# Kernel optimization log

Measured on AMD Instinct MI355X. Metric: run time of the kernel, lower is better.

Reference implementation:

```python
import jax, jax.numpy as jnp
import numpy as np

# irreps_in = irreps_out = "32x0e + 16x1o"; irreps_edge = "1x0e + 1x1o"
N_SCAL, N_VEC = 32, 16
RADIAL_EMBED, HIDDEN = 64, 64
# FullyConnectedTensorProduct instructions (uvw), v == 1 since edge mults are 1:
#  P1: 0e x 0e -> 0e (32*32)   P2: 1o x 1o -> 0e (16*32)
#  P3: 0e x 1o -> 1o (32*16)   P4: 1o x 0e -> 1o (16*16)   P5: 1o x 1o -> 1o (16*16)
SPLITS = np.cumsum([0, 32 * 32, 16 * 32, 32 * 16, 16 * 16, 16 * 16])
W_NUMEL = int(SPLITS[-1])  # 2560
SILU_NORM = 1.6790425  # e3nn normalize2mom constant for silu
# path weights: alpha = ir_out.dim / sum(num_elements over paths into same output)
PW0 = (1.0 / (32.0 + 16.0)) ** 0.5          # scalar output paths
PW1 = (3.0 / (32.0 + 16.0 + 16.0)) ** 0.5   # vector output paths
INV_SQRT3 = 3.0 ** -0.5  # wigner_3j(0,1,1)/(1,0,1)/(1,1,0) magnitude
INV_SQRT6 = 6.0 ** -0.5  # wigner_3j(1,1,1) = eps_ijk / sqrt(6)
N_NODES, N_EDGES = 8192, 65536


def radial_net(e, W0, W1, W2):
    # e3nn FullyConnectedNet: x @ (W / sqrt(fan_in)), normalized silu between layers
    h = e
    for W in (W0, W1):
        h = jax.nn.silu(h @ (W / jnp.sqrt(jnp.float32(W.shape[0])))) * SILU_NORM
    return h @ (W2 / jnp.sqrt(jnp.float32(W2.shape[0])))


def setup_inputs() -> dict:
    key = jax.random.key(0)
    ks = jax.random.split(key, 9)
    edge_index = jax.random.randint(ks[0], (2, N_EDGES), 0, N_NODES)
    node_feat = jax.random.normal(ks[1], (N_NODES, N_SCAL + 3 * N_VEC), jnp.float32)
    edge_feat = jax.random.normal(ks[2], (N_EDGES, 4), jnp.float32)
    edge_embed = jax.random.normal(ks[3], (N_EDGES, RADIAL_EMBED), jnp.float32)
    W_fc0 = jax.random.normal(ks[4], (RADIAL_EMBED, HIDDEN), jnp.float32)
    W_fc1 = jax.random.normal(ks[5], (HIDDEN, HIDDEN), jnp.float32)
    W_fc2 = jax.random.normal(ks[6], (HIDDEN, W_NUMEL), jnp.float32)
    Wsc0 = jax.random.normal(ks[7], (N_SCAL, N_SCAL), jnp.float32)
    Wsc1 = jax.random.normal(ks[8], (N_VEC, N_VEC), jnp.float32)
    return dict(edge_index=edge_index, node_feat=node_feat, edge_feat=edge_feat,
                edge_embed=edge_embed, dim_size=N_NODES,
                W_fc0=W_fc0, W_fc1=W_fc1, W_fc2=W_fc2, Wsc0=Wsc0, Wsc1=Wsc1)


def reference(edge_index, node_feat, edge_feat, edge_embed, dim_size,
              W_fc0, W_fc1, W_fc2, Wsc0, Wsc1):
    src, dst = edge_index[0], edge_index[1]
    w = radial_net(edge_embed, W_fc0, W_fc1, W_fc2)  # [E, 2560]
    W1 = w[:, SPLITS[0]:SPLITS[1]].reshape(-1, 32, 32)
    W2 = w[:, SPLITS[1]:SPLITS[2]].reshape(-1, 16, 32)
    W3 = w[:, SPLITS[2]:SPLITS[3]].reshape(-1, 32, 16)
    W4 = w[:, SPLITS[3]:SPLITS[4]].reshape(-1, 16, 16)
    W5 = w[:, SPLITS[4]:SPLITS[5]].reshape(-1, 16, 16)
    xe = node_feat[src]                                    # gather [E, 80]
    x0 = xe[:, :N_SCAL]                                    # [E, 32]
    x1 = xe[:, N_SCAL:].reshape(-1, N_VEC, 3)              # [E, 16, 3]
    y0, y1 = edge_feat[:, 0], edge_feat[:, 1:4]            # [E], [E, 3]
    # scalar outputs
    dot = jnp.einsum('eui,ei->eu', x1, y1)
    out0 = PW0 * (jnp.einsum('euw,eu,e->ew', W1, x0, y0)
                  + INV_SQRT3 * jnp.einsum('euw,eu->ew', W2, dot))
    # vector outputs ((x cross y)_k = eps_ijk x_i y_j)
    cross = jnp.cross(x1, y1[:, None, :])
    out1 = PW1 * (INV_SQRT3 * jnp.einsum('euw,eu,ek->ewk', W3, x0, y1)
                  + INV_SQRT3 * jnp.einsum('euw,euk,e->ewk', W4, x1, y0)
                  + INV_SQRT6 * jnp.einsum('euw,euk->ewk', W5, cross))
    msg = jnp.concatenate([out0, out1.reshape(-1, 3 * N_VEC)], axis=1)  # [E, 80]
    agg = jax.ops.segment_sum(msg, dst, num_segments=dim_size)          # [N, 80]
    # self-connection: e3nn o3.Linear applied per irrep, / sqrt(fan_in)
    n0 = node_feat[:, :N_SCAL]
    n1 = node_feat[:, N_SCAL:].reshape(-1, N_VEC, 3)
    sc0 = n0 @ Wsc0 / jnp.sqrt(jnp.float32(N_SCAL))
    sc1 = jnp.einsum('nui,uv->nvi', n1, Wsc1) / jnp.sqrt(jnp.float32(N_VEC))
    sc = jnp.concatenate([sc0, sc1.reshape(-1, 3 * N_VEC)], axis=1)
    return agg + sc
```

## Files before the change

kernel.cpp:

```cpp
#include <hip/hip_runtime.h>

typedef unsigned short u16;
typedef __bf16 bf16x8 __attribute__((ext_vector_type(8)));
typedef float  f32x4  __attribute__((ext_vector_type(4)));

#define NEDGES 65536
#define NNODES 8192

#define PW0f       0.14433756729740643f
#define PW1f       0.21650635094610965f
#define INV_SQRT3f 0.5773502691896258f
#define INV_SQRT6f 0.4082482904638631f
#define SILU_NORMf 1.6790425f

#define WT2_OFF 0
#define WT0_OFF 163840
#define WT1_OFF 167936
#define WS_ELEMS 172032

#define HSTR 72

__device__ __forceinline__ float silu_n(float z) {
    return SILU_NORMf * z / (1.0f + __expf(-z));
}
__device__ __forceinline__ u16 f2bf(float f) {
    return __builtin_bit_cast(u16, (__bf16)f);
}
__device__ __forceinline__ float bf2f(u16 u) {
    unsigned v = ((unsigned)u) << 16;
    return __builtin_bit_cast(float, v);
}
__device__ __forceinline__ bf16x8 ld_bf8(const u16* p) {
    return *reinterpret_cast<const bf16x8*>(p);
}
__device__ __forceinline__ bf16x8 cvt_bf8(const float* p) {
    float4 a = *reinterpret_cast<const float4*>(p);
    float4 b = *reinterpret_cast<const float4*>(p + 4);
    bf16x8 r;
    r[0]=(__bf16)a.x; r[1]=(__bf16)a.y; r[2]=(__bf16)a.z; r[3]=(__bf16)a.w;
    r[4]=(__bf16)b.x; r[5]=(__bf16)b.y; r[6]=(__bf16)b.z; r[7]=(__bf16)b.w;
    return r;
}
#define MFMA16(A,B,C) __builtin_amdgcn_mfma_f32_16x16x32_bf16(A,B,C,0,0,0)

__global__ void k_prep(const float* __restrict__ Wfc0,
                       const float* __restrict__ Wfc1,
                       const float* __restrict__ Wfc2,
                       const float* __restrict__ node_feat,
                       const float* __restrict__ Wsc0,
                       const float* __restrict__ Wsc1,
                       u16* __restrict__ ws,
                       float* __restrict__ out)
{
    const int bid = blockIdx.x;
    if (bid < 672) {
        int gid = bid * 256 + threadIdx.x;
        if (gid < 163840) {
            int k = gid / 2560;
            int j = gid - k * 2560;
            float s;
            if (j < 1024)      s = PW0f;
            else if (j < 1536) s = PW0f * INV_SQRT3f;
            else if (j < 2304) s = PW1f * INV_SQRT3f;
            else               s = PW1f * INV_SQRT6f;
            ws[WT2_OFF + j * 64 + k] = f2bf(Wfc2[gid] * (0.125f * s));
        } else if (gid < WT1_OFF) {
            int i = gid - WT0_OFF;
            int k = i >> 6, n = i & 63;
            ws[WT0_OFF + n * 64 + k] = f2bf(Wfc0[i] * 0.125f);
        } else if (gid < WS_ELEMS) {
            int i = gid - WT1_OFF;
            int k = i >> 6, n = i & 63;
            ws[WT1_OFF + n * 64 + k] = f2bf(Wfc1[i] * 0.125f);
        }
    } else {
        int gid = (bid - 672) * 256 + threadIdx.x;
        if (gid >= NNODES * 80) return;
        int n = gid / 80;
        int s = gid - n * 80;
        const float* nf = node_feat + (size_t)n * 80;
        float r;
        if (s < 32) {
            float a = 0.f;
            #pragma unroll
            for (int u = 0; u < 32; ++u) a += nf[u] * Wsc0[u * 32 + s];
            r = a * 0.17677669529663687f;
        } else {
            int v = (s - 32) / 3;
            int k = (s - 32) - v * 3;
            float a = 0.f;
            #pragma unroll
            for (int u = 0; u < 16; ++u) a += nf[32 + u * 3 + k] * Wsc1[u * 16 + v];
            r = a * 0.25f;
        }
        out[gid] = r;
    }
}

__global__ __launch_bounds__(256, 3) void k_main(
    const int*   __restrict__ eidx,
    const float* __restrict__ node_feat,
    const float* __restrict__ edge_feat,
    const float* __restrict__ edge_embed,
    const u16*   __restrict__ ws,
    float*       __restrict__ out)
{
    __shared__ __align__(16) char smem[40192];
    u16*   h1S   = (u16*)(smem);
    u16*   c12S  = (u16*)(smem + 9216);
    u16*   coefB = (u16*)(smem + 15360);
    int*   dstS  = (int*)(smem + 39936);
    u16*   h0S   = (u16*)(smem + 15360);
    float* msgS  = (float*)(smem + 9216);

    const int t    = threadIdx.x;
    const int lane = t & 63;
    const int l15  = lane & 15;
    const int lq   = lane >> 4;
    const int wid  = t >> 6;
    const int role = (wid + blockIdx.x) & 3;
    const int eg0  = blockIdx.x * 64;

    const u16* WT2 = ws + WT2_OFF;
    const u16* WT0 = ws + WT0_OFF;
    const u16* WT1 = ws + WT1_OFF;

    {
        const float* erow = edge_embed + (size_t)(eg0 + wid * 16 + l15) * 64 + 8 * lq;
        bf16x8 eB0 = cvt_bf8(erow);
        bf16x8 eB1 = cvt_bf8(erow + 32);
        #pragma unroll
        for (int ntl = 0; ntl < 4; ++ntl) {
            const u16* a = WT0 + (ntl * 16 + l15) * 64 + 8 * lq;
            bf16x8 A0 = ld_bf8(a);
            bf16x8 A1 = ld_bf8(a + 32);
            f32x4 z = {0.f, 0.f, 0.f, 0.f};
            z = MFMA16(A0, eB0, z);
            f32x4 dd = MFMA16(A1, eB1, z);
            ushort4 pk;
            pk.x = f2bf(silu_n(dd[0]));
            pk.y = f2bf(silu_n(dd[1]));
            pk.z = f2bf(silu_n(dd[2]));
            pk.w = f2bf(silu_n(dd[3]));
            *(ushort4*)&h0S[(wid * 16 + l15) * HSTR + ntl * 16 + lq * 4] = pk;
        }
    }
    {
        const u16* hrow = h0S + (wid * 16 + l15) * HSTR + 8 * lq;
        bf16x8 hB0 = ld_bf8(hrow);
        bf16x8 hB1 = ld_bf8(hrow + 32);
        #pragma unroll
        for (int ntl = 0; ntl < 4; ++ntl) {
            const u16* a = WT1 + (ntl * 16 + l15) * 64 + 8 * lq;
            bf16x8 A0 = ld_bf8(a);
            bf16x8 A1 = ld_bf8(a + 32);
            f32x4 z = {0.f, 0.f, 0.f, 0.f};
            z = MFMA16(A0, hB0, z);
            f32x4 dd = MFMA16(A1, hB1, z);
            ushort4 pk;
            pk.x = f2bf(silu_n(dd[0]));
            pk.y = f2bf(silu_n(dd[1]));
            pk.z = f2bf(silu_n(dd[2]));
            pk.w = f2bf(silu_n(dd[3]));
            *(ushort4*)&h1S[(wid * 16 + l15) * HSTR + ntl * 16 + lq * 4] = pk;
        }
    }
    __syncthreads();

    {
        const int e   = t & 63;
        const int q   = t >> 6;
        const int eg  = eg0 + e;
        const int src = eidx[eg];
        const float* nf = node_feat + (size_t)src * 80;
        const float* ef = edge_feat + (size_t)eg * 4;
        if (q == 0) {
            dstS[e] = eidx[NEDGES + eg];
            const float y0 = ef[0];
            #pragma unroll
            for (int u = 0; u < 32; ++u) c12S[u * 64 + e] = f2bf(nf[u] * y0);
        } else if (q == 1) {
            const float ya = ef[1], yb = ef[2], yc = ef[3];
            #pragma unroll
            for (int u = 0; u < 16; ++u) {
                float d = nf[32 + u * 3] * ya + nf[32 + u * 3 + 1] * yb
                        + nf[32 + u * 3 + 2] * yc;
                c12S[(32 + u) * 64 + e] = f2bf(d);
            }
        } else if (q == 2) {
            const float ya = ef[1], yb = ef[2], yc = ef[3];
            #pragma unroll
            for (int u = 0; u < 32; ++u) {
                const float x = nf[u];
                coefB[(u * 3 + 0) * 64 + e] = f2bf(x * ya);
                coefB[(u * 3 + 1) * 64 + e] = f2bf(x * yb);
                coefB[(u * 3 + 2) * 64 + e] = f2bf(x * yc);
            }
        } else {
            const float y0 = ef[0], ya = ef[1], yb = ef[2], yc = ef[3];
            #pragma unroll
            for (int u = 0; u < 16; ++u) {
                const float xa = nf[32 + u * 3], xb = nf[32 + u * 3 + 1], xc = nf[32 + u * 3 + 2];
                coefB[(96 + u * 3 + 0) * 64 + e] = f2bf(xa * y0);
                coefB[(96 + u * 3 + 1) * 64 + e] = f2bf(xb * y0);
                coefB[(96 + u * 3 + 2) * 64 + e] = f2bf(xc * y0);
                coefB[(144 + u * 3 + 0) * 64 + e] = f2bf(xb * yc - xc * yb);
                coefB[(144 + u * 3 + 1) * 64 + e] = f2bf(xc * ya - xa * yc);
                coefB[(144 + u * 3 + 2) * 64 + e] = f2bf(xa * yb - xb * ya);
            }
        }
    }
    __syncthreads();

    bf16x8 hb[4][2];
    #pragma unroll
    for (int eg = 0; eg < 4; ++eg) {
        const u16* r = h1S + (eg * 16 + l15) * HSTR + 8 * lq;
        hb[eg][0] = ld_bf8(r);
        hb[eg][1] = ld_bf8(r + 32);
    }

    float acc[48];
    #pragma unroll
    for (int i = 0; i < 48; ++i) acc[i] = 0.f;

    int t0, ntile;
    if (role < 2) { t0 = role * 48;            ntile = 48; }
    else          { t0 = 96 + (role - 2) * 32; ntile = 32; }

    const u16* Aw = WT2 + l15 * 64 + 8 * lq;

#define COMPUTE(A0_, A1_, D_)                                          \
    {                                                                  \
        _Pragma("unroll")                                              \
        for (int eg = 0; eg < 4; ++eg) {                               \
            f32x4 z = {0.f, 0.f, 0.f, 0.f};                            \
            z = MFMA16(A0_, hb[eg][0], z);                             \
            D_[eg] = MFMA16(A1_, hb[eg][1], z);                        \
        }                                                              \
    }

#define EPILOGUE(D_, TT_, HS_)                                              \
    {                                                                       \
        if (role < 2) {                                                     \
            const u16* cr = c12S + ((TT_) >> 1) * 64;                       \
            _Pragma("unroll")                                               \
            for (int eg = 0; eg < 4; ++eg) {                                \
                const float c = bf2f(cr[eg * 16 + l15]);                    \
                _Pragma("unroll")                                           \
                for (int r = 0; r < 4; ++r)                                 \
                    acc[eg * 8 + (HS_) * 4 + r] += c * D_[eg][r];           \
            }                                                               \
        } else {                                                            \
            const u16* cr = coefB + ((TT_) - 96) * 192;                     \
            _Pragma("unroll")                                               \
            for (int eg = 0; eg < 4; ++eg) {                                \
                const int e16 = eg * 16 + l15;                              \
                const float c0 = bf2f(cr[e16]);                             \
                const float c1 = bf2f(cr[64 + e16]);                        \
                const float c2 = bf2f(cr[128 + e16]);                       \
                _Pragma("unroll")                                           \
                for (int r = 0; r < 4; ++r) {                               \
                    const float dv = D_[eg][r];                             \
                    acc[eg * 12 + r * 3 + 0] += c0 * dv;                    \
                    acc[eg * 12 + r * 3 + 1] += c1 * dv;                    \
                    acc[eg * 12 + r * 3 + 2] += c2 * dv;                    \
                }                                                           \
            }                                                               \
        }                                                                   \
    }

    bf16x8 Aa0, Aa1, Ab0, Ab1;
    {
        const u16* p = Aw + (size_t)t0 * 1024;
        Aa0 = ld_bf8(p); Aa1 = ld_bf8(p + 32);
        const u16* q = Aw + (size_t)(t0 + 1) * 1024;
        Ab0 = ld_bf8(q); Ab1 = ld_bf8(q + 32);
    }
    const int np = ntile >> 1;
    #pragma unroll 1
    for (int p = 0; p < np; ++p) {
        const int tt = t0 + 2 * p;
        bf16x8 Ac0, Ac1, Ad0, Ad1;
        const bool more = (p + 1 < np);
        if (more) {
            const u16* q = Aw + (size_t)(tt + 2) * 1024;
            Ac0 = ld_bf8(q); Ac1 = ld_bf8(q + 32);
        }
        f32x4 d[4];
        COMPUTE(Aa0, Aa1, d);
        EPILOGUE(d, tt, 0);
        if (more) {
            const u16* q = Aw + (size_t)(tt + 3) * 1024;
            Ad0 = ld_bf8(q); Ad1 = ld_bf8(q + 32);
        }
        COMPUTE(Ab0, Ab1, d);
        EPILOGUE(d, tt + 1, 1);
        if (more) { Aa0 = Ac0; Aa1 = Ac1; Ab0 = Ad0; Ab1 = Ad1; }
    }
#undef COMPUTE
#undef EPILOGUE

    __syncthreads();
    if (role == 0) {
        #pragma unroll
        for (int eg = 0; eg < 4; ++eg) {
            float* mb = msgS + (eg * 16 + l15) * 81;
            #pragma unroll
            for (int hs = 0; hs < 2; ++hs)
                #pragma unroll
                for (int r = 0; r < 4; ++r)
                    mb[hs * 16 + lq * 4 + r] = acc[eg * 8 + hs * 4 + r];
        }
    } else if (role == 2) {
        #pragma unroll
        for (int eg = 0; eg < 4; ++eg) {
            float* mb = msgS + (eg * 16 + l15) * 81 + 32;
            #pragma unroll
            for (int r = 0; r < 4; ++r)
                #pragma unroll
                for (int k = 0; k < 3; ++k)
                    mb[(lq * 4 + r) * 3 + k] = acc[eg * 12 + r * 3 + k];
        }
    }
    __syncthreads();
    if (role == 1) {
        #pragma unroll
        for (int eg = 0; eg < 4; ++eg) {
            float* mb = msgS + (eg * 16 + l15) * 81;
            #pragma unroll
            for (int hs = 0; hs < 2; ++hs)
                #pragma unroll
                for (int r = 0; r < 4; ++r)
                    mb[hs * 16 + lq * 4 + r] += acc[eg * 8 + hs * 4 + r];
        }
    } else if (role == 3) {
        #pragma unroll
        for (int eg = 0; eg < 4; ++eg) {
            float* mb = msgS + (eg * 16 + l15) * 81 + 32;
            #pragma unroll
            for (int r = 0; r < 4; ++r)
                #pragma unroll
                for (int k = 0; k < 3; ++k)
                    mb[(lq * 4 + r) * 3 + k] += acc[eg * 12 + r * 3 + k];
        }
    }
    __syncthreads();

    for (int idx = t; idx < 64 * 81; idx += 256) {
        const int e = idx / 81;
        const int s = idx - e * 81;
        if (s < 80)
            atomicAdd(out + (size_t)dstS[e] * 80 + s, msgS[idx]);
    }
}

extern "C" void kernel_launch(void* const* d_in, const int* in_sizes, int n_in,
                              void* d_out, int out_size, void* d_ws, size_t ws_size,
                              hipStream_t stream) {
    const int*   eidx       = (const int*)d_in[0];
    const float* node_feat  = (const float*)d_in[1];
    const float* edge_feat  = (const float*)d_in[2];
    const float* edge_embed = (const float*)d_in[3];
    const float* Wfc0       = (const float*)d_in[5];
    const float* Wfc1       = (const float*)d_in[6];
    const float* Wfc2       = (const float*)d_in[7];
    const float* Wsc0       = (const float*)d_in[8];
    const float* Wsc1       = (const float*)d_in[9];
    float* out = (float*)d_out;
    u16*   ws  = (u16*)d_ws;

    if (ws_size < (size_t)WS_ELEMS * sizeof(u16)) return;

    hipLaunchKernelGGL(k_prep, dim3(672 + 2560), dim3(256), 0, stream,
                       Wfc0, Wfc1, Wfc2, node_feat, Wsc0, Wsc1, ws, out);
    hipLaunchKernelGGL(k_main, dim3(NEDGES / 64), dim3(256), 0, stream,
                       eidx, node_feat, edge_feat, edge_embed, ws, out);
}
```

Baseline: 93.64 us.

## Factor P3 path out of per-edge GEMM, halve edges per block, overlap MLP and gather

The 0e x 1o -> 1o path is restructured: instead of expanding x0*y1 into 96 coefficient rows, it contracts W3 with x0 once per output and multiplies by y1 in the epilogue, cutting that path's MFMA tiles from 96 to 32. Edges per block drop from 64 to 32 with 4 blocks per CU, shrinking shared memory and accumulator registers. The radial MLP now runs on two waves while the other two gather node features, removing one barrier. Smaller tiles raise per-block weight reloads of WT2 and atomic overhead per block stays similar.

```diff
diff --git a/kernel.cpp b/kernel.cpp
--- a/kernel.cpp
+++ b/kernel.cpp
@@ -6,6 +6,7 @@
 
 #define NEDGES 65536
 #define NNODES 8192
+#define EPB 32
 
 #define PW0f       0.14433756729740643f
 #define PW1f       0.21650635094610965f
@@ -97,7 +98,7 @@
     }
 }
 
-__global__ __launch_bounds__(256, 3) void k_main(
+__global__ __launch_bounds__(256, 4) void k_main(
     const int*   __restrict__ eidx,
     const float* __restrict__ node_feat,
     const float* __restrict__ edge_feat,
@@ -105,13 +106,15 @@
     const u16*   __restrict__ ws,
     float*       __restrict__ out)
 {
-    __shared__ __align__(16) char smem[40192];
-    u16*   h1S   = (u16*)(smem);
-    u16*   c12S  = (u16*)(smem + 9216);
-    u16*   coefB = (u16*)(smem + 15360);
-    int*   dstS  = (int*)(smem + 39936);
-    u16*   h0S   = (u16*)(smem + 15360);
-    float* msgS  = (float*)(smem + 9216);
+    __shared__ __align__(16) char smem[20992];
+    u16*   h1S  = (u16*)(smem);
+    u16*   h0S  = (u16*)(smem + 4608);
+    u16*   c12S = (u16*)(smem + 9216);
+    u16*   x0S  = (u16*)(smem + 12288);
+    u16*   cw45 = (u16*)(smem + 14336);
+    float* y1S  = (float*)(smem + 20480);
+    int*   dstS = (int*)(smem + 20864);
+    float* msgS = (float*)(smem + 4608);
 
     const int t    = threadIdx.x;
     const int lane = t & 63;
@@ -119,13 +122,13 @@
     const int lq   = lane >> 4;
     const int wid  = t >> 6;
     const int role = (wid + blockIdx.x) & 3;
-    const int eg0  = blockIdx.x * 64;
+    const int eg0  = blockIdx.x * EPB;
 
     const u16* WT2 = ws + WT2_OFF;
-    const u16* WT0 = ws + WT0_OFF;
-    const u16* WT1 = ws + WT1_OFF;
-
-    {
+
+    if (wid < 2) {
+        const u16* WT0 = ws + WT0_OFF;
+        const u16* WT1 = ws + WT1_OFF;
         const float* erow = edge_embed + (size_t)(eg0 + wid * 16 + l15) * 64 + 8 * lq;
         bf16x8 eB0 = cvt_bf8(erow);
         bf16x8 eB1 = cvt_bf8(erow + 32);
@@ -144,8 +147,6 @@
             pk.w = f2bf(silu_n(dd[3]));
             *(ushort4*)&h0S[(wid * 16 + l15) * HSTR + ntl * 16 + lq * 4] = pk;
         }
-    }
-    {
         const u16* hrow = h0S + (wid * 16 + l15) * HSTR + 8 * lq;
         bf16x8 hB0 = ld_bf8(hrow);
         bf16x8 hB1 = ld_bf8(hrow + 32);
@@ -164,12 +165,10 @@
             pk.w = f2bf(silu_n(dd[3]));
             *(ushort4*)&h1S[(wid * 16 + l15) * HSTR + ntl * 16 + lq * 4] = pk;
         }
-    }
-    __syncthreads();
-
-    {
-        const int e   = t & 63;
-        const int q   = t >> 6;
+    } else {
+        const int t2  = t - 128;
+        const int e   = t2 & 31;
+        const int q   = t2 >> 5;
         const int eg  = eg0 + e;
         const int src = eidx[eg];
         const float* nf = node_feat + (size_t)src * 80;
@@ -177,97 +176,107 @@
         if (q == 0) {
             dstS[e] = eidx[NEDGES + eg];
             const float y0 = ef[0];
-            #pragma unroll
-            for (int u = 0; u < 32; ++u) c12S[u * 64 + e] = f2bf(nf[u] * y0);
+            y1S[e] = ef[1]; y1S[32 + e] = ef[2]; y1S[64 + e] = ef[3];
+            #pragma unroll
+            for (int u = 0; u < 32; ++u) c12S[u * 32 + e] = f2bf(nf[u] * y0);
         } else if (q == 1) {
             const float ya = ef[1], yb = ef[2], yc = ef[3];
             #pragma unroll
             for (int u = 0; u < 16; ++u) {
                 float d = nf[32 + u * 3] * ya + nf[32 + u * 3 + 1] * yb
                         + nf[32 + u * 3 + 2] * yc;
-                c12S[(32 + u) * 64 + e] = f2bf(d);
+                c12S[(32 + u) * 32 + e] = f2bf(d);
             }
+            #pragma unroll
+            for (int u = 0; u < 32; ++u) x0S[u * 32 + e] = f2bf(nf[u]);
         } else if (q == 2) {
-            const float ya = ef[1], yb = ef[2], yc = ef[3];
-            #pragma unroll
-            for (int u = 0; u < 32; ++u) {
-                const float x = nf[u];
-                coefB[(u * 3 + 0) * 64 + e] = f2bf(x * ya);
-                coefB[(u * 3 + 1) * 64 + e] = f2bf(x * yb);
-                coefB[(u * 3 + 2) * 64 + e] = f2bf(x * yc);
+            const float y0 = ef[0];
+            #pragma unroll
+            for (int u = 0; u < 16; ++u) {
+                cw45[(u * 3 + 0) * 32 + e] = f2bf(nf[32 + u * 3 + 0] * y0);
+                cw45[(u * 3 + 1) * 32 + e] = f2bf(nf[32 + u * 3 + 1] * y0);
+                cw45[(u * 3 + 2) * 32 + e] = f2bf(nf[32 + u * 3 + 2] * y0);
             }
         } else {
-            const float y0 = ef[0], ya = ef[1], yb = ef[2], yc = ef[3];
+            const float ya = ef[1], yb = ef[2], yc = ef[3];
             #pragma unroll
             for (int u = 0; u < 16; ++u) {
                 const float xa = nf[32 + u * 3], xb = nf[32 + u * 3 + 1], xc = nf[32 + u * 3 + 2];
-                coefB[(96 + u * 3 + 0) * 64 + e] = f2bf(xa * y0);
-                coefB[(96 + u * 3 + 1) * 64 + e] = f2bf(xb * y0);
-                coefB[(96 + u * 3 + 2) * 64 + e] = f2bf(xc * y0);
-                coefB[(144 + u * 3 + 0) * 64 + e] = f2bf(xb * yc - xc * yb);
-                coefB[(144 + u * 3 + 1) * 64 + e] = f2bf(xc * ya - xa * yc);
-                coefB[(144 + u * 3 + 2) * 64 + e] = f2bf(xa * yb - xb * ya);
+                cw45[(48 + u * 3 + 0) * 32 + e] = f2bf(xb * yc - xc * yb);
+                cw45[(48 + u * 3 + 1) * 32 + e] = f2bf(xc * ya - xa * yc);
+                cw45[(48 + u * 3 + 2) * 32 + e] = f2bf(xa * yb - xb * ya);
             }
         }
     }
     __syncthreads();
 
-    bf16x8 hb[4][2];
+    bf16x8 hb[2][2];
     #pragma unroll
-    for (int eg = 0; eg < 4; ++eg) {
+    for (int eg = 0; eg < 2; ++eg) {
         const u16* r = h1S + (eg * 16 + l15) * HSTR + 8 * lq;
         hb[eg][0] = ld_bf8(r);
         hb[eg][1] = ld_bf8(r + 32);
     }
 
-    float acc[48];
+    float acc[32];
     #pragma unroll
-    for (int i = 0; i < 48; ++i) acc[i] = 0.f;
+    for (int i = 0; i < 32; ++i) acc[i] = 0.f;
 
     int t0, ntile;
-    if (role < 2) { t0 = role * 48;            ntile = 48; }
-    else          { t0 = 96 + (role - 2) * 32; ntile = 32; }
+    if      (role == 0) { t0 = 0;   ntile = 48; }
+    else if (role == 1) { t0 = 48;  ntile = 48; }
+    else if (role == 2) { t0 = 96;  ntile = 40; }
+    else                { t0 = 136; ntile = 24; }
 
     const u16* Aw = WT2 + l15 * 64 + 8 * lq;
 
 #define COMPUTE(A0_, A1_, D_)                                          \
     {                                                                  \
         _Pragma("unroll")                                              \
-        for (int eg = 0; eg < 4; ++eg) {                               \
+        for (int eg = 0; eg < 2; ++eg) {                               \
             f32x4 z = {0.f, 0.f, 0.f, 0.f};                            \
             z = MFMA16(A0_, hb[eg][0], z);                             \
             D_[eg] = MFMA16(A1_, hb[eg][1], z);                        \
         }                                                              \
     }
 
-#define EPILOGUE(D_, TT_, HS_)                                              \
-    {                                                                       \
-        if (role < 2) {                                                     \
-            const u16* cr = c12S + ((TT_) >> 1) * 64;                       \
-            _Pragma("unroll")                                               \
-            for (int eg = 0; eg < 4; ++eg) {                                \
-                const float c = bf2f(cr[eg * 16 + l15]);                    \
-                _Pragma("unroll")                                           \
-                for (int r = 0; r < 4; ++r)                                 \
-                    acc[eg * 8 + (HS_) * 4 + r] += c * D_[eg][r];           \
-            }                                                               \
-        } else {                                                            \
-            const u16* cr = coefB + ((TT_) - 96) * 192;                     \
-            _Pragma("unroll")                                               \
-            for (int eg = 0; eg < 4; ++eg) {                                \
-                const int e16 = eg * 16 + l15;                              \
-                const float c0 = bf2f(cr[e16]);                             \
-                const float c1 = bf2f(cr[64 + e16]);                        \
-                const float c2 = bf2f(cr[128 + e16]);                       \
-                _Pragma("unroll")                                           \
-                for (int r = 0; r < 4; ++r) {                               \
-                    const float dv = D_[eg][r];                             \
-                    acc[eg * 12 + r * 3 + 0] += c0 * dv;                    \
-                    acc[eg * 12 + r * 3 + 1] += c1 * dv;                    \
-                    acc[eg * 12 + r * 3 + 2] += c2 * dv;                    \
-                }                                                           \
-            }                                                               \
-        }                                                                   \
+#define EPILOGUE(D_, TT_, HS_)                                               \
+    {                                                                        \
+        if ((TT_) < 96) {                         \
+            const u16* cr = c12S + ((TT_) >> 1) * 32;                        \
+            _Pragma("unroll")                                                \
+            for (int eg = 0; eg < 2; ++eg) {                                 \
+                const float c = bf2f(cr[eg * 16 + l15]);                     \
+                _Pragma("unroll")                                            \
+                for (int r = 0; r < 4; ++r)                                  \
+                    acc[eg * 8 + (HS_) * 4 + r] += c * D_[eg][r];            \
+            }                                                                \
+        } else if ((TT_) < 128) {             \
+            const u16* cr = x0S + ((TT_) - 96) * 32;                         \
+            _Pragma("unroll")                                                \
+            for (int eg = 0; eg < 2; ++eg) {                                 \
+                const float c = bf2f(cr[eg * 16 + l15]);                     \
+                _Pragma("unroll")                                            \
+                for (int r = 0; r < 4; ++r)                                  \
+                    acc[24 + eg * 4 + r] += c * D_[eg][r];                   \
+            }                                                                \
+        } else {                                   \
+            const u16* cr = cw45 + ((TT_) - 128) * 96;                       \
+            _Pragma("unroll")                                                \
+            for (int eg = 0; eg < 2; ++eg) {                                 \
+                const int e16 = eg * 16 + l15;                               \
+                const float c0 = bf2f(cr[e16]);                              \
+                const float c1 = bf2f(cr[32 + e16]);                         \
+                const float c2 = bf2f(cr[64 + e16]);                         \
+                _Pragma("unroll")                                            \
+                for (int r = 0; r < 4; ++r) {                                \
+                    const float dv = D_[eg][r];                              \
+                    acc[eg * 12 + r * 3 + 0] += c0 * dv;                     \
+                    acc[eg * 12 + r * 3 + 1] += c1 * dv;                     \
+                    acc[eg * 12 + r * 3 + 2] += c2 * dv;                     \
+                }                                                            \
+            }                                                                \
+        }                                                                    \
     }
 
     bf16x8 Aa0, Aa1, Ab0, Ab1;
@@ -287,7 +296,7 @@
             const u16* q = Aw + (size_t)(tt + 2) * 1024;
             Ac0 = ld_bf8(q); Ac1 = ld_bf8(q + 32);
         }
-        f32x4 d[4];
+        f32x4 d[2];
         COMPUTE(Aa0, Aa1, d);
         EPILOGUE(d, tt, 0);
         if (more) {
@@ -304,7 +313,7 @@
     __syncthreads();
     if (role == 0) {
         #pragma unroll
-        for (int eg = 0; eg < 4; ++eg) {
+        for (int eg = 0; eg < 2; ++eg) {
             float* mb = msgS + (eg * 16 + l15) * 81;
             #pragma unroll
             for (int hs = 0; hs < 2; ++hs)
@@ -314,19 +323,23 @@
         }
     } else if (role == 2) {
         #pragma unroll
-        for (int eg = 0; eg < 4; ++eg) {
-            float* mb = msgS + (eg * 16 + l15) * 81 + 32;
-            #pragma unroll
-            for (int r = 0; r < 4; ++r)
-                #pragma unroll
-                for (int k = 0; k < 3; ++k)
-                    mb[(lq * 4 + r) * 3 + k] = acc[eg * 12 + r * 3 + k];
+        for (int eg = 0; eg < 2; ++eg) {
+            const int e = eg * 16 + l15;
+            const float w1x = y1S[e], w1y = y1S[32 + e], w1z = y1S[64 + e];
+            float* mb = msgS + e * 81 + 32;
+            #pragma unroll
+            for (int r = 0; r < 4; ++r) {
+                const float s = acc[24 + eg * 4 + r];
+                mb[(lq * 4 + r) * 3 + 0] = acc[eg * 12 + r * 3 + 0] + s * w1x;
+                mb[(lq * 4 + r) * 3 + 1] = acc[eg * 12 + r * 3 + 1] + s * w1y;
+                mb[(lq * 4 + r) * 3 + 2] = acc[eg * 12 + r * 3 + 2] + s * w1z;
+            }
         }
     }
     __syncthreads();
     if (role == 1) {
         #pragma unroll
-        for (int eg = 0; eg < 4; ++eg) {
+        for (int eg = 0; eg < 2; ++eg) {
             float* mb = msgS + (eg * 16 + l15) * 81;
             #pragma unroll
             for (int hs = 0; hs < 2; ++hs)
@@ -336,7 +349,7 @@
         }
     } else if (role == 3) {
         #pragma unroll
-        for (int eg = 0; eg < 4; ++eg) {
+        for (int eg = 0; eg < 2; ++eg) {
             float* mb = msgS + (eg * 16 + l15) * 81 + 32;
             #pragma unroll
             for (int r = 0; r < 4; ++r)
@@ -347,11 +360,10 @@
     }
     __syncthreads();
 
-    for (int idx = t; idx < 64 * 81; idx += 256) {
-        const int e = idx / 81;
-        const int s = idx - e * 81;
-        if (s < 80)
-            atomicAdd(out + (size_t)dstS[e] * 80 + s, msgS[idx]);
+    for (int idx = t; idx < EPB * 80; idx += 256) {
+        const int e = idx / 80;
+        const int s = idx - e * 80;
+        atomicAdd(out + (size_t)dstS[e] * 80 + s, msgS[e * 81 + s]);
     }
 }
 
@@ -374,6 +386,6 @@
 
     hipLaunchKernelGGL(k_prep, dim3(672 + 2560), dim3(256), 0, stream,
                        Wfc0, Wfc1, Wfc2, node_feat, Wsc0, Wsc1, ws, out);
-    hipLaunchKernelGGL(k_main, dim3(NEDGES / 64), dim3(256), 0, stream,
+    hipLaunchKernelGGL(k_main, dim3(NEDGES / EPB), dim3(256), 0, stream,
                        eidx, node_feat, edge_feat, edge_embed, ws, out);
 }
```

After: 110.0 us. 1.17x slower.

## Replace atomic scatter with CSR-sorted edge messages and per-node gather

Applied to the files above, without the earlier changes.

Instead of scattering each edge message into the output with float atomics, the main kernel writes messages to a workspace buffer. A counting sort (count, scan, fill kernels) builds per-destination edge lists, and a gather kernel sums each node's messages and adds them to the self-connection output. This removes 5.2M global float atomics, at the cost of four extra launches, a serial single-block scan, a 21MB message buffer round-trip, and a nondeterministic edge order within each node. It falls back to the old path if the workspace is too small.

```diff
diff --git a/kernel.cpp b/kernel.cpp
--- a/kernel.cpp
+++ b/kernel.cpp
@@ -6,6 +6,7 @@
 
 #define NEDGES 65536
 #define NNODES 8192
+#define EPB 64
 
 #define PW0f       0.14433756729740643f
 #define PW1f       0.21650635094610965f
@@ -17,6 +18,13 @@
 #define WT0_OFF 163840
 #define WT1_OFF 167936
 #define WS_ELEMS 172032
+
+#define OFF_CNT   344064
+#define OFF_OFS   376832
+#define OFF_CUR   409856
+#define OFF_ELIST 442624
+#define OFF_MSG   704768
+#define WS_NEED   21676288
 
 #define HSTR 72
 
@@ -43,13 +51,20 @@
 }
 #define MFMA16(A,B,C) __builtin_amdgcn_mfma_f32_16x16x32_bf16(A,B,C,0,0,0)
 
+__global__ void k_zero(int* __restrict__ cnt) {
+    int i = blockIdx.x * 256 + threadIdx.x;
+    if (i < NNODES) cnt[i] = 0;
+}
+
 __global__ void k_prep(const float* __restrict__ Wfc0,
                        const float* __restrict__ Wfc1,
                        const float* __restrict__ Wfc2,
                        const float* __restrict__ node_feat,
                        const float* __restrict__ Wsc0,
                        const float* __restrict__ Wsc1,
+                       const int*   __restrict__ eidx,
                        u16* __restrict__ ws,
+                       int* __restrict__ cnt,
                        float* __restrict__ out)
 {
     const int bid = blockIdx.x;
@@ -73,7 +88,7 @@
             int k = i >> 6, n = i & 63;
             ws[WT1_OFF + n * 64 + k] = f2bf(Wfc1[i] * 0.125f);
         }
-    } else {
+    } else if (bid < 3232) {
         int gid = (bid - 672) * 256 + threadIdx.x;
         if (gid >= NNODES * 80) return;
         int n = gid / 80;
@@ -94,15 +109,56 @@
             r = a * 0.25f;
         }
         out[gid] = r;
-    }
-}
-
+    } else {
+        int e = (bid - 3232) * 256 + threadIdx.x;
+        if (e < NEDGES) atomicAdd(&cnt[eidx[NEDGES + e]], 1);
+    }
+}
+
+__global__ __launch_bounds__(1024) void k_scan(const int* __restrict__ cnt,
+                                               int* __restrict__ ofs,
+                                               int* __restrict__ cur)
+{
+    __shared__ int ps[1024];
+    const int t = threadIdx.x;
+    const int base = t * 8;
+    int v[8]; int s = 0;
+    #pragma unroll
+    for (int i = 0; i < 8; ++i) { v[i] = cnt[base + i]; s += v[i]; }
+    ps[t] = s;
+    __syncthreads();
+    int acc = s;
+    for (int off = 1; off < 1024; off <<= 1) {
+        int x = (t >= off) ? ps[t - off] : 0;
+        __syncthreads();
+        acc += x;
+        ps[t] = acc;
+        __syncthreads();
+    }
+    int run = acc - s;
+    #pragma unroll
+    for (int i = 0; i < 8; ++i) { ofs[base + i] = run; cur[base + i] = run; run += v[i]; }
+    if (t == 1023) ofs[NNODES] = run;
+}
+
+__global__ void k_fill(const int* __restrict__ eidx,
+                       int* __restrict__ cur,
+                       int* __restrict__ elist)
+{
+    int e = blockIdx.x * 256 + threadIdx.x;
+    int d = eidx[NEDGES + e];
+    int pos = atomicAdd(&cur[d], 1);
+    elist[pos] = e;
+}
+
+template<int TAIL>
 __global__ __launch_bounds__(256, 3) void k_main(
     const int*   __restrict__ eidx,
     const float* __restrict__ node_feat,
     const float* __restrict__ edge_feat,
     const float* __restrict__ edge_embed,
     const u16*   __restrict__ ws,
+    float*       __restrict__ msgbuf,
     float*       __restrict__ out)
 {
     __shared__ __align__(16) char smem[40192];
@@ -119,7 +175,7 @@
     const int lq   = lane >> 4;
     const int wid  = t >> 6;
     const int role = (wid + blockIdx.x) & 3;
-    const int eg0  = blockIdx.x * 64;
+    const int eg0  = blockIdx.x * EPB;
 
     const u16* WT2 = ws + WT2_OFF;
     const u16* WT0 = ws + WT0_OFF;
@@ -347,12 +403,48 @@
     }
     __syncthreads();
 
-    for (int idx = t; idx < 64 * 81; idx += 256) {
-        const int e = idx / 81;
-        const int s = idx - e * 81;
-        if (s < 80)
-            atomicAdd(out + (size_t)dstS[e] * 80 + s, msgS[idx]);
-    }
+    if (TAIL == 1) {
+        float* mrow = msgbuf + (size_t)eg0 * 80;
+        for (int idx = t; idx < EPB * 80; idx += 256) {
+            const int e = idx / 80;
+            const int s = idx - e * 80;
+            mrow[idx] = msgS[e * 81 + s];
+        }
+    } else {
+        for (int idx = t; idx < 64 * 81; idx += 256) {
+            const int e = idx / 81;
+            const int s = idx - e * 81;
+            if (s < 80)
+                atomicAdd(out + (size_t)dstS[e] * 80 + s, msgS[idx]);
+        }
+    }
+}
+
+__global__ __launch_bounds__(256) void k_gather(const int* __restrict__ ofs,
+                                                const int* __restrict__ elist,
+                                                const float* __restrict__ msg,
+                                                float* __restrict__ out)
+{
+    const int lane = threadIdx.x & 63;
+    const int n = blockIdx.x * 4 + (threadIdx.x >> 6);
+    const int jb = ofs[n], je = ofs[n + 1];
+    float v0 = 0.f, v1 = 0.f;
+    int j = jb;
+    for (; j + 2 <= je; j += 2) {
+        const int e0 = elist[j], e1 = elist[j + 1];
+        const float* m0 = msg + (size_t)e0 * 80;
+        const float* m1 = msg + (size_t)e1 * 80;
+        v0 += m0[lane] + m1[lane];
+        if (lane < 16) v1 += m0[64 + lane] + m1[64 + lane];
+    }
+    if (j < je) {
+        const float* m0 = msg + (size_t)elist[j] * 80;
+        v0 += m0[lane];
+        if (lane < 16) v1 += m0[64 + lane];
+    }
+    float* op = out + (size_t)n * 80;
+    op[lane] += v0;
+    if (lane < 16) op[64 + lane] += v1;
 }
 
 extern "C" void kernel_launch(void* const* d_in, const int* in_sizes, int n_in,
@@ -368,12 +460,33 @@
     const float* Wsc0       = (const float*)d_in[8];
     const float* Wsc1       = (const float*)d_in[9];
     float* out = (float*)d_out;
+    char*  wsb = (char*)d_ws;
     u16*   ws  = (u16*)d_ws;
 
     if (ws_size < (size_t)WS_ELEMS * sizeof(u16)) return;
 
-    hipLaunchKernelGGL(k_prep, dim3(672 + 2560), dim3(256), 0, stream,
-                       Wfc0, Wfc1, Wfc2, node_feat, Wsc0, Wsc1, ws, out);
-    hipLaunchKernelGGL(k_main, dim3(NEDGES / 64), dim3(256), 0, stream,
-                       eidx, node_feat, edge_feat, edge_embed, ws, out);
-}
+    const bool big = ws_size >= (size_t)WS_NEED;
+    int*   cnt    = (int*)(wsb + OFF_CNT);
+    int*   ofs    = (int*)(wsb + OFF_OFS);
+    int*   cur    = (int*)(wsb + OFF_CUR);
+    int*   elist  = (int*)(wsb + OFF_ELIST);
+    float* msgbuf = (float*)(wsb + OFF_MSG);
+
+    if (big) {
+        hipLaunchKernelGGL(k_zero, dim3(32), dim3(256), 0, stream, cnt);
+        hipLaunchKernelGGL(k_prep, dim3(3488), dim3(256), 0, stream,
+                           Wfc0, Wfc1, Wfc2, node_feat, Wsc0, Wsc1, eidx, ws, cnt, out);
+        hipLaunchKernelGGL(k_scan, dim3(1), dim3(1024), 0, stream, cnt, ofs, cur);
+        hipLaunchKernelGGL(k_fill, dim3(NEDGES / 256), dim3(256), 0, stream,
+                           eidx, cur, elist);
+        hipLaunchKernelGGL((k_main<1>), dim3(NEDGES / EPB), dim3(256), 0, stream,
+                           eidx, node_feat, edge_feat, edge_embed, ws, msgbuf, out);
+        hipLaunchKernelGGL(k_gather, dim3(NNODES / 4), dim3(256), 0, stream,
+                           ofs, elist, msgbuf, out);
+    } else {
+        hipLaunchKernelGGL(k_prep, dim3(3232), dim3(256), 0, stream,
+                           Wfc0, Wfc1, Wfc2, node_feat, Wsc0, Wsc1, eidx, ws, cnt, out);
+        hipLaunchKernelGGL((k_main<0>), dim3(NEDGES / EPB), dim3(256), 0, stream,
+                           eidx, node_feat, edge_feat, edge_embed, ws, msgbuf, out);
+    }
+}
```

Result: slower. 102.9 us (+9.9%).
